# Performance work log

Measured on AMD Instinct MI355X. Metric: run time of the kernel, lower is better.

The kernel has to match this reference:

```python
import jax, jax.numpy as jnp
import numpy as np

# PtConv dims from SegSmall: pl=64 channels, n_centers=16 kernel elements, dim=3
B, N, K = 4, 16384, 16          # batch, points, neighbors
C_IN, C_OUT, KS, DIM = 64, 64, 16, 3


def setup_inputs() -> dict:
    key = jax.random.key(0)
    ks = jax.random.split(key, 10)
    features = jax.random.normal(ks[0], (B, N, C_IN), dtype=jnp.float32)
    input_pts = jax.random.uniform(ks[1], (B, N, DIM), dtype=jnp.float32)
    output_pts = input_pts  # same-resolution conv: queries == input points
    indices = jax.random.randint(ks[2], (B, N, K), 0, N)  # precomputed KNN indices
    # weight init as in PtConv
    bound = float(np.sqrt(3.0) * np.sqrt(2.0 / (C_IN + C_OUT)))
    weight = jax.random.uniform(ks[3], (C_IN, KS, C_OUT), jnp.float32, -bound, bound)
    bias = jnp.zeros((C_OUT,), jnp.float32)
    centers = jax.random.uniform(ks[4], (DIM, KS), jnp.float32, -1.0, 1.0)
    # position-MLP params: Linear(dim*KS -> 2*KS), Linear(2*KS -> KS), Linear(KS -> KS)
    def lin(k, fan_in, fan_out):
        lim = 1.0 / np.sqrt(fan_in)
        kw, kb = jax.random.split(k)
        W = jax.random.uniform(kw, (fan_in, fan_out), jnp.float32, -lim, lim)
        b = jax.random.uniform(kb, (fan_out,), jnp.float32, -lim, lim)
        return W, b
    w1, b1 = lin(ks[5], DIM * KS, 2 * KS)
    w2, b2 = lin(ks[6], 2 * KS, KS)
    w3, b3 = lin(ks[7], KS, KS)
    return {"features": features, "input_pts": input_pts, "output_pts": output_pts,
            "weight": weight, "bias": bias, "centers": centers,
            "w1": w1, "b1": b1, "w2": w2, "b2": b2, "w3": w3, "b3": b3,
            "indices": indices}


def reference(features, input_pts, output_pts, weight, bias, centers,
              w1, b1, w2, b2, w3, b3, indices):
    # per-batch gather of neighbor features and coordinates
    gather = jax.vmap(lambda a, idx: a[idx])
    feat_g = gather(features, indices)          # [B, M, K, C_in]
    pts_g = gather(input_pts, indices)          # [B, M, K, 3]
    pts = pts_g - output_pts[:, :, None, :]      # nn_center=True
    # distances to kernel centers: [B,M,K,3,1] - [3,KS] -> [B,M,K,3,KS] -> [B,M,K,3*KS]
    d = (pts[..., None] - centers).reshape(pts.shape[0], pts.shape[1], pts.shape[2], -1)
    d = jax.nn.relu(d @ w1 + b1)
    d = jax.nn.relu(d @ w2 + b2)
    d = jax.nn.relu(d @ w3 + b3)                 # [B, M, K, KS]
    # weighted neighbor aggregation: bmm(features^T, dists)
    agg = jnp.einsum('bmkc,bmkj->bmcj', feat_g, d)   # [B, M, C_in, KS]
    out = jnp.einsum('bmcj,cjo->bmo', agg, weight)   # flatten (C_in,KS) matches weight.view(-1,out)
    out = out / feat_g.shape[2]                      # divide by K (fs[2])
    out = out + bias
    return out
```

## Files before the change

kernel.cpp:

```cpp
#include <hip/hip_runtime.h>

#define NPTS 16384
#define KN   16
#define CIN  64
#define COUT 64
#define KSIZ 16
#define PTS  16

typedef _Float16 h4v    __attribute__((ext_vector_type(4)));
typedef _Float16 h8v    __attribute__((ext_vector_type(8)));
typedef __fp16   fp16x2 __attribute__((ext_vector_type(2)));
typedef float    f32x4  __attribute__((ext_vector_type(4)));

union H2U { fp16x2 h; unsigned u; };
union H4U { h4v v; fp16x2 p[2]; uint2 u2; };
union H8U { h8v v; uint4 u4; };

#define WS_WF_OFF   512
#define WS_F16_OFF  131584
#define WS_NEEDED   (131584ull + 8388608ull)

__global__ void prep_kernel(const float* __restrict__ weight,
                            const float* __restrict__ w1,
                            const float* __restrict__ b1,
                            const float* __restrict__ centers,
                            const float* __restrict__ features,
                            unsigned* __restrict__ wsp,
                            uint4* __restrict__ wf,
                            uint4* __restrict__ fb16) {
    const int b = blockIdx.x;
    const int t = threadIdx.x;
    if (b < 32) {
        const int bp = b*4 + (t>>6);
        const int kk = bp >> 2, nt = bp & 3;
        const int l = t & 63, li = l & 15, g = l >> 4;
        unsigned short u[8];
        #pragma unroll
        for (int e = 0; e < 8; ++e) {
            int s = kk*32 + g*8 + e;
            int j = s >> 6;
            int c = s & 63;
            union { _Float16 h; unsigned short s16; } cv;
            cv.h = (_Float16)(weight[(c*16 + j)*64 + nt*16 + li] * 0.0625f);
            u[e] = cv.s16;
        }
        uint4 v;
        v.x = u[0] | ((unsigned)u[1] << 16);
        v.y = u[2] | ((unsigned)u[3] << 16);
        v.z = u[4] | ((unsigned)u[5] << 16);
        v.w = u[6] | ((unsigned)u[7] << 16);
        wf[(kk*4 + nt)*64 + l] = v;
    } else if (b == 32) {
        __shared__ float tmp[4][32];
        if (t < 32) {
            int n = t;
            float s0 = 0.f, s1 = 0.f, s2 = 0.f, bf = b1[n];
            for (int s = 0; s < KSIZ; ++s) {
                float a0 = w1[(0*KSIZ + s)*32 + n];
                float a1 = w1[(1*KSIZ + s)*32 + n];
                float a2 = w1[(2*KSIZ + s)*32 + n];
                s0 += a0; s1 += a1; s2 += a2;
                bf -= centers[0*KSIZ+s]*a0 + centers[1*KSIZ+s]*a1 + centers[2*KSIZ+s]*a2;
            }
            tmp[0][n] = s0; tmp[1][n] = s1; tmp[2][n] = s2; tmp[3][n] = bf;
        }
        __syncthreads();
        if (t < 64) {
            const int row = t >> 4, q = t & 15;
            union { _Float16 h[2]; unsigned u; } pk;
            pk.h[0] = (_Float16)tmp[row][2*q];
            pk.h[1] = (_Float16)tmp[row][2*q+1];
            wsp[row*16 + q] = pk.u;
        }
    } else {
        const size_t e0 = ((size_t)(b - 33)*256 + t) * 8;
        const float4 f0 = *(const float4*)(features + e0);
        const float4 f1 = *(const float4*)(features + e0 + 4);
        union { _Float16 h[8]; uint4 v; } o;
        o.h[0] = (_Float16)f0.x; o.h[1] = (_Float16)f0.y;
        o.h[2] = (_Float16)f0.z; o.h[3] = (_Float16)f0.w;
        o.h[4] = (_Float16)f1.x; o.h[5] = (_Float16)f1.y;
        o.h[6] = (_Float16)f1.z; o.h[7] = (_Float16)f1.w;
        fb16[e0 >> 3] = o.v;
    }
}

template<int FM>
__global__ __launch_bounds__(256, 5)
void ptconv_kernel(const float* __restrict__ features,
                   const float* __restrict__ input_pts,
                   const float* __restrict__ output_pts,
                   const float* __restrict__ bias,
                   const float* __restrict__ w2,
                   const float* __restrict__ b2,
                   const float* __restrict__ w3,
                   const float* __restrict__ b3,
                   const int*   __restrict__ indices,
                   const unsigned* __restrict__ folded,
                   const uint4* __restrict__ wf,
                   const uint2* __restrict__ fb16,
                   float* __restrict__ out) {
    __shared__ __align__(16) char smem[32768];
    char* s_agg = smem;

    const int t    = threadIdx.x;
    const int l    = t & 63;
    const int wave = t >> 6;
    const int li   = l & 15;
    const int g    = l >> 4;
    const int m0   = blockIdx.x * PTS;
    const int bbk  = m0 >> 14;
    const int mloc = m0 & (NPTS-1);

    const int*   idxB  = indices    + (size_t)bbk*NPTS*KN;
    const float* ptsB  = input_pts  + (size_t)bbk*NPTS*3;
    const float* optsB = output_pts + (size_t)bbk*NPTS*3;
    const float* fb    = features + (size_t)bbk*NPTS*CIN;
    const uint2* fb16B = fb16 + (size_t)bbk*NPTS*(CIN/4);

    const int p1 = t >> 4, k1 = t & 15;
    const int nn = mloc + p1;
    const int idxv = idxB[nn*KN + k1];
    const float cop0 = optsB[nn*3+0], cop1 = optsB[nn*3+1], cop2 = optsB[nn*3+2];
    const float cip0 = ptsB[(size_t)idxv*3+0];
    const float cip1 = ptsB[(size_t)idxv*3+1];
    const float cip2 = ptsB[(size_t)idxv*3+2];

    const int4 idA = *(const int4*)(idxB + (mloc + wave*4+0)*KN + 4*g);
    const int4 idB = *(const int4*)(idxB + (mloc + wave*4+1)*KN + 4*g);
    const int4 idC = *(const int4*)(idxB + (mloc + wave*4+2)*KN + 4*g);
    const int4 idD = *(const int4*)(idxB + (mloc + wave*4+3)*KN + 4*g);

    H4U gA0, gA1, gA2, gA3, gB0, gB1, gB2, gB3;
    H4U gC0, gC1, gC2, gC3, gD0, gD1, gD2, gD3;
    f32x4 fA0, fA1, fA2, fA3, fB0, fB1, fB2, fB3;
    if constexpr (FM == 1) {
        gA0.u2 = fb16B[(size_t)idA.x*16 + li]; gA1.u2 = fb16B[(size_t)idA.y*16 + li];
        gA2.u2 = fb16B[(size_t)idA.z*16 + li]; gA3.u2 = fb16B[(size_t)idA.w*16 + li];
        gB0.u2 = fb16B[(size_t)idB.x*16 + li]; gB1.u2 = fb16B[(size_t)idB.y*16 + li];
        gB2.u2 = fb16B[(size_t)idB.z*16 + li]; gB3.u2 = fb16B[(size_t)idB.w*16 + li];
        gC0.u2 = fb16B[(size_t)idC.x*16 + li]; gC1.u2 = fb16B[(size_t)idC.y*16 + li];
        gC2.u2 = fb16B[(size_t)idC.z*16 + li]; gC3.u2 = fb16B[(size_t)idC.w*16 + li];
        gD0.u2 = fb16B[(size_t)idD.x*16 + li]; gD1.u2 = fb16B[(size_t)idD.y*16 + li];
        gD2.u2 = fb16B[(size_t)idD.z*16 + li]; gD3.u2 = fb16B[(size_t)idD.w*16 + li];
    } else {
        fA0 = *(const f32x4*)(fb + (size_t)idA.x*CIN + 4*li);
        fA1 = *(const f32x4*)(fb + (size_t)idA.y*CIN + 4*li);
        fA2 = *(const f32x4*)(fb + (size_t)idA.z*CIN + 4*li);
        fA3 = *(const f32x4*)(fb + (size_t)idA.w*CIN + 4*li);
        fB0 = *(const f32x4*)(fb + (size_t)idB.x*CIN + 4*li);
        fB1 = *(const f32x4*)(fb + (size_t)idB.y*CIN + 4*li);
        fB2 = *(const f32x4*)(fb + (size_t)idB.z*CIN + 4*li);
        fB3 = *(const f32x4*)(fb + (size_t)idB.w*CIN + 4*li);
    }

    h8v w2f; h4v w3f;
    #pragma unroll
    for (int e = 0; e < 8; ++e) w2f[e] = (_Float16)w2[(8*g+e)*16 + li];
    #pragma unroll
    for (int e = 0; e < 4; ++e) w3f[e] = (_Float16)w3[(4*g+e)*16 + li];
    const f32x4 b2v4  = *(const f32x4*)(b2 + 4*g);
    const float b3v   = b3[li];
    const float biasO = bias[wave*16 + li];
    const uint4* wp   = wf + wave*64 + l;

    {
        const __fp16 r0h = (__fp16)(cip0-cop0);
        const __fp16 r1h = (__fp16)(cip1-cop1);
        const __fp16 r2h = (__fp16)(cip2-cop2);
        fp16x2 r0p = {r0h, r0h}, r1p = {r1h, r1h}, r2p = {r2h, r2h};
        const fp16x2 zz = {(__fp16)0.f, (__fp16)0.f};
        uint4* dst = (uint4*)(smem + wave*8192 + l*80);
        unsigned o8[8];
        #pragma unroll
        for (int half = 0; half < 2; ++half) {
            #pragma unroll
            for (int qq = 0; qq < 8; ++qq) {
                const int q = half*8 + qq;
                H2U a, u0, u1, u2;
                a.u  = folded[48+q];
                u0.u = folded[q];
                u1.u = folded[16+q];
                u2.u = folded[32+q];
                fp16x2 acc = r0p*u0.h + a.h;
                acc = r1p*u1.h + acc;
                acc = r2p*u2.h + acc;
                acc = __builtin_elementwise_max(acc, zz);
                H2U o; o.h = acc; o8[qq] = o.u;
            }
            dst[half*2+0] = make_uint4(o8[0], o8[1], o8[2], o8[3]);
            dst[half*2+1] = make_uint4(o8[4], o8[5], o8[6], o8[7]);
        }
    }

    h4v dreg0, dreg1, dreg2, dreg3;
#define L23(PP, DREG) { \
    h8v B2 = *(const h8v*)(smem + wave*8192 + ((PP)*16 + li)*80 + g*16); \
    f32x4 a2 = b2v4; \
    a2 = __builtin_amdgcn_mfma_f32_16x16x32_f16(w2f, B2, a2, 0, 0, 0); \
    H4U A3; \
    A3.p[0] = __builtin_amdgcn_cvt_pkrtz(fmaxf(a2[0],0.f), fmaxf(a2[1],0.f)); \
    A3.p[1] = __builtin_amdgcn_cvt_pkrtz(fmaxf(a2[2],0.f), fmaxf(a2[3],0.f)); \
    f32x4 a3 = {b3v, b3v, b3v, b3v}; \
    a3 = __builtin_amdgcn_mfma_f32_16x16x16f16(A3.v, w3f, a3, 0, 0, 0); \
    H4U Dv; \
    Dv.p[0] = __builtin_amdgcn_cvt_pkrtz(fmaxf(a3[0],0.f), fmaxf(a3[1],0.f)); \
    Dv.p[1] = __builtin_amdgcn_cvt_pkrtz(fmaxf(a3[2],0.f), fmaxf(a3[3],0.f)); \
    DREG = Dv.v; }
    L23(0, dreg0) L23(1, dreg1) L23(2, dreg2) L23(3, dreg3)
#undef L23

#define P2STORE(PP, E0,E1,E2,E3) { \
    const int pix_ = wave*4 + (PP); \
    const unsigned swz_ = (unsigned)((pix_ & 7) << 4); \
    char* ab_ = s_agg + pix_*2048; \
    _Pragma("unroll") \
    for (int r = 0; r < 4; ++r) { \
        H2U d01, d23; \
        d01.h = __builtin_amdgcn_cvt_pkrtz(E0[r], E1[r]); \
        d23.h = __builtin_amdgcn_cvt_pkrtz(E2[r], E3[r]); \
        *(uint2*)(ab_ + ((unsigned)((4*g + r)*128 + 8*li) ^ swz_)) = \
            make_uint2(d01.u, d23.u); \
    } }

    if constexpr (FM == 1) {
#define P2F16(PP, R0,R1,R2,R3) { \
        f32x4 z = {0.f,0.f,0.f,0.f}; \
        f32x4 e0_, e1_, e2_, e3_; \
        { H4U B_; B_.v = (h4v){R0.v[0], R1.v[0], R2.v[0], R3.v[0]}; \
          e0_ = __builtin_amdgcn_mfma_f32_16x16x16f16(dreg##PP, B_.v, z, 0, 0, 0); } \
        { H4U B_; B_.v = (h4v){R0.v[1], R1.v[1], R2.v[1], R3.v[1]}; \
          e1_ = __builtin_amdgcn_mfma_f32_16x16x16f16(dreg##PP, B_.v, z, 0, 0, 0); } \
        { H4U B_; B_.v = (h4v){R0.v[2], R1.v[2], R2.v[2], R3.v[2]}; \
          e2_ = __builtin_amdgcn_mfma_f32_16x16x16f16(dreg##PP, B_.v, z, 0, 0, 0); } \
        { H4U B_; B_.v = (h4v){R0.v[3], R1.v[3], R2.v[3], R3.v[3]}; \
          e3_ = __builtin_amdgcn_mfma_f32_16x16x16f16(dreg##PP, B_.v, z, 0, 0, 0); } \
        P2STORE(PP, e0_, e1_, e2_, e3_) }
        P2F16(0, gA0, gA1, gA2, gA3)
        P2F16(1, gB0, gB1, gB2, gB3)
        P2F16(2, gC0, gC1, gC2, gC3)
        P2F16(3, gD0, gD1, gD2, gD3)
#undef P2F16
    } else {
#define P2F32(PP, R0,R1,R2,R3) { \
        f32x4 z = {0.f,0.f,0.f,0.f}; \
        f32x4 e0_, e1_, e2_, e3_; \
        { H4U B_; B_.p[0] = __builtin_amdgcn_cvt_pkrtz(R0[0], R1[0]); \
          B_.p[1] = __builtin_amdgcn_cvt_pkrtz(R2[0], R3[0]); \
          e0_ = __builtin_amdgcn_mfma_f32_16x16x16f16(dreg##PP, B_.v, z, 0, 0, 0); } \
        { H4U B_; B_.p[0] = __builtin_amdgcn_cvt_pkrtz(R0[1], R1[1]); \
          B_.p[1] = __builtin_amdgcn_cvt_pkrtz(R2[1], R3[1]); \
          e1_ = __builtin_amdgcn_mfma_f32_16x16x16f16(dreg##PP, B_.v, z, 0, 0, 0); } \
        { H4U B_; B_.p[0] = __builtin_amdgcn_cvt_pkrtz(R0[2], R1[2]); \
          B_.p[1] = __builtin_amdgcn_cvt_pkrtz(R2[2], R3[2]); \
          e2_ = __builtin_amdgcn_mfma_f32_16x16x16f16(dreg##PP, B_.v, z, 0, 0, 0); } \
        { H4U B_; B_.p[0] = __builtin_amdgcn_cvt_pkrtz(R0[3], R1[3]); \
          B_.p[1] = __builtin_amdgcn_cvt_pkrtz(R2[3], R3[3]); \
          e3_ = __builtin_amdgcn_mfma_f32_16x16x16f16(dreg##PP, B_.v, z, 0, 0, 0); } \
        P2STORE(PP, e0_, e1_, e2_, e3_) }
        P2F32(0, fA0, fA1, fA2, fA3)
        P2F32(1, fB0, fB1, fB2, fB3)
        fA0 = *(const f32x4*)(fb + (size_t)idC.x*CIN + 4*li);
        fA1 = *(const f32x4*)(fb + (size_t)idC.y*CIN + 4*li);
        fA2 = *(const f32x4*)(fb + (size_t)idC.z*CIN + 4*li);
        fA3 = *(const f32x4*)(fb + (size_t)idC.w*CIN + 4*li);
        fB0 = *(const f32x4*)(fb + (size_t)idD.x*CIN + 4*li);
        fB1 = *(const f32x4*)(fb + (size_t)idD.y*CIN + 4*li);
        fB2 = *(const f32x4*)(fb + (size_t)idD.z*CIN + 4*li);
        fB3 = *(const f32x4*)(fb + (size_t)idD.w*CIN + 4*li);
        P2F32(2, fA0, fA1, fA2, fA3)
        P2F32(3, fB0, fB1, fB2, fB3)
#undef P2F32
    }
#undef P2STORE

    uint4 q0 = wp[0*256], q1 = wp[1*256], q2 = wp[2*256], q3 = wp[3*256];
    uint4 q4 = wp[4*256], q5 = wp[5*256], q6 = wp[6*256], q7 = wp[7*256];

    asm volatile("s_waitcnt lgkmcnt(0)" ::: "memory");
    __builtin_amdgcn_s_barrier();
    asm volatile("" ::: "memory");

    __builtin_amdgcn_s_setprio(1);
    f32x4 a0 = {0.f,0.f,0.f,0.f}, a1 = a0, a2 = a0, a3 = a0;
    const unsigned swr = (unsigned)((li & 7) << 4);
#define AREAD(KK) (*(const h8v*)(s_agg + li*2048 + (((KK)*64 + g*16) ^ swr)))
#define MFS(KK, Q, ACC)  { H8U bu_; bu_.u4 = Q; \
    ACC = __builtin_amdgcn_mfma_f32_16x16x32_f16(AREAD(KK), bu_.v, ACC, 0, 0, 0); }
#define MFSL(KK, Q, ACC) MFS(KK, Q, ACC) Q = wp[((KK)+8)*256];
    MFSL(0, q0, a0) MFSL(1, q1, a1) MFSL(2, q2, a2) MFSL(3, q3, a3)
    MFSL(4, q4, a0) MFSL(5, q5, a1) MFSL(6, q6, a2) MFSL(7, q7, a3)
    MFSL(8, q0, a0) MFSL(9, q1, a1) MFSL(10, q2, a2) MFSL(11, q3, a3)
    MFSL(12, q4, a0) MFSL(13, q5, a1) MFSL(14, q6, a2) MFSL(15, q7, a3)
    MFSL(16, q0, a0) MFSL(17, q1, a1) MFSL(18, q2, a2) MFSL(19, q3, a3)
    MFSL(20, q4, a0) MFSL(21, q5, a1) MFSL(22, q6, a2) MFSL(23, q7, a3)
    MFS(24, q0, a0) MFS(25, q1, a1) MFS(26, q2, a2) MFS(27, q3, a3)
    MFS(28, q4, a0) MFS(29, q5, a1) MFS(30, q6, a2) MFS(31, q7, a3)
#undef MFSL
#undef MFS
#undef AREAD
    __builtin_amdgcn_s_setprio(0);

    const f32x4 acc = (a0 + a1) + (a2 + a3);
    #pragma unroll
    for (int r = 0; r < 4; ++r) {
        const int mr = g*4 + r;
        out[(size_t)(m0 + mr)*COUT + wave*16 + li] = acc[r] + biasO;
    }
}

extern "C" void kernel_launch(void* const* d_in, const int* in_sizes, int n_in,
                              void* d_out, int out_size, void* d_ws, size_t ws_size,
                              hipStream_t stream) {
    const float* features   = (const float*)d_in[0];
    const float* input_pts  = (const float*)d_in[1];
    const float* output_pts = (const float*)d_in[2];
    const float* weight     = (const float*)d_in[3];
    const float* bias       = (const float*)d_in[4];
    const float* centers    = (const float*)d_in[5];
    const float* w1         = (const float*)d_in[6];
    const float* b1         = (const float*)d_in[7];
    const float* w2         = (const float*)d_in[8];
    const float* b2         = (const float*)d_in[9];
    const float* w3         = (const float*)d_in[10];
    const float* b3         = (const float*)d_in[11];
    const int*   indices    = (const int*)d_in[12];
    float* out = (float*)d_out;
    unsigned* wsp = (unsigned*)d_ws;
    uint4* wf   = (uint4*)((char*)d_ws + WS_WF_OFF);
    uint4* fb16 = (uint4*)((char*)d_ws + WS_F16_OFF);

    const bool f16ok = ws_size >= WS_NEEDED;
    const int nconv = f16ok ? (4*NPTS*CIN) / (256*8) : 0;
    prep_kernel<<<33 + nconv, 256, 0, stream>>>(
        weight, w1, b1, centers, features, wsp, wf, fb16);

    const int total_pts = 4 * NPTS;
    if (f16ok) {
        ptconv_kernel<1><<<total_pts / PTS, 256, 0, stream>>>(
            features, input_pts, output_pts, bias,
            w2, b2, w3, b3, indices, wsp, wf, (const uint2*)fb16, out);
    } else {
        ptconv_kernel<0><<<total_pts / PTS, 256, 0, stream>>>(
            features, input_pts, output_pts, bias,
            w2, b2, w3, b3, indices, wsp, wf, (const uint2*)fb16, out);
    }
}
```

Measured before the change: 48.21 us.

## Make fp16 kernel persistent over four tiles with software-pipelined neighbor prefetch

The fp16 path now has each block handle four consecutive 16-point tiles instead of one, launching a quarter as many blocks. Indices, positions and gathered fp16 features for the next tile are loaded during the current tile's compute, hiding gather latency and amortising per-block setup (w2/w3/bias loads). This costs an extra barrier per tile, more live registers, a lower launch-bounds occupancy target (4 instead of 5) and fewer blocks to spread across CUs. The fp32 fallback is split into its own kernel and behaves as before.

```diff
diff --git a/kernel.cpp b/kernel.cpp
--- a/kernel.cpp
+++ b/kernel.cpp
@@ -6,6 +6,7 @@
 #define COUT 64
 #define KSIZ 16
 #define PTS  16
+#define ITERS 4
 
 typedef _Float16 h4v    __attribute__((ext_vector_type(4)));
 typedef _Float16 h8v    __attribute__((ext_vector_type(8)));
@@ -85,21 +86,19 @@
     }
 }
 
-template<int FM>
-__global__ __launch_bounds__(256, 5)
-void ptconv_kernel(const float* __restrict__ features,
-                   const float* __restrict__ input_pts,
-                   const float* __restrict__ output_pts,
-                   const float* __restrict__ bias,
-                   const float* __restrict__ w2,
-                   const float* __restrict__ b2,
-                   const float* __restrict__ w3,
-                   const float* __restrict__ b3,
-                   const int*   __restrict__ indices,
-                   const unsigned* __restrict__ folded,
-                   const uint4* __restrict__ wf,
-                   const uint2* __restrict__ fb16,
-                   float* __restrict__ out) {
+__global__ __launch_bounds__(256, 4)
+void ptconv_pipe(const float* __restrict__ input_pts,
+                 const float* __restrict__ output_pts,
+                 const float* __restrict__ bias,
+                 const float* __restrict__ w2,
+                 const float* __restrict__ b2,
+                 const float* __restrict__ w3,
+                 const float* __restrict__ b3,
+                 const int*   __restrict__ indices,
+                 const unsigned* __restrict__ folded,
+                 const uint4* __restrict__ wf,
+                 const uint2* __restrict__ fb16,
+                 float* __restrict__ out) {
     __shared__ __align__(16) char smem[32768];
     char* s_agg = smem;
 
@@ -108,51 +107,15 @@
     const int wave = t >> 6;
     const int li   = l & 15;
     const int g    = l >> 4;
-    const int m0   = blockIdx.x * PTS;
-    const int bbk  = m0 >> 14;
-    const int mloc = m0 & (NPTS-1);
+    const int base_m0 = blockIdx.x * (PTS*ITERS);
+    const int bbk   = base_m0 >> 14;
+    const int mloc  = base_m0 & (NPTS-1);
+    const int p1 = t >> 4, k1 = t & 15;
 
     const int*   idxB  = indices    + (size_t)bbk*NPTS*KN;
     const float* ptsB  = input_pts  + (size_t)bbk*NPTS*3;
     const float* optsB = output_pts + (size_t)bbk*NPTS*3;
-    const float* fb    = features + (size_t)bbk*NPTS*CIN;
     const uint2* fb16B = fb16 + (size_t)bbk*NPTS*(CIN/4);
-
-    const int p1 = t >> 4, k1 = t & 15;
-    const int nn = mloc + p1;
-    const int idxv = idxB[nn*KN + k1];
-    const float cop0 = optsB[nn*3+0], cop1 = optsB[nn*3+1], cop2 = optsB[nn*3+2];
-    const float cip0 = ptsB[(size_t)idxv*3+0];
-    const float cip1 = ptsB[(size_t)idxv*3+1];
-    const float cip2 = ptsB[(size_t)idxv*3+2];
-
-    const int4 idA = *(const int4*)(idxB + (mloc + wave*4+0)*KN + 4*g);
-    const int4 idB = *(const int4*)(idxB + (mloc + wave*4+1)*KN + 4*g);
-    const int4 idC = *(const int4*)(idxB + (mloc + wave*4+2)*KN + 4*g);
-    const int4 idD = *(const int4*)(idxB + (mloc + wave*4+3)*KN + 4*g);
-
-    H4U gA0, gA1, gA2, gA3, gB0, gB1, gB2, gB3;
-    H4U gC0, gC1, gC2, gC3, gD0, gD1, gD2, gD3;
-    f32x4 fA0, fA1, fA2, fA3, fB0, fB1, fB2, fB3;
-    if constexpr (FM == 1) {
-        gA0.u2 = fb16B[(size_t)idA.x*16 + li]; gA1.u2 = fb16B[(size_t)idA.y*16 + li];
-        gA2.u2 = fb16B[(size_t)idA.z*16 + li]; gA3.u2 = fb16B[(size_t)idA.w*16 + li];
-        gB0.u2 = fb16B[(size_t)idB.x*16 + li]; gB1.u2 = fb16B[(size_t)idB.y*16 + li];
-        gB2.u2 = fb16B[(size_t)idB.z*16 + li]; gB3.u2 = fb16B[(size_t)idB.w*16 + li];
-        gC0.u2 = fb16B[(size_t)idC.x*16 + li]; gC1.u2 = fb16B[(size_t)idC.y*16 + li];
-        gC2.u2 = fb16B[(size_t)idC.z*16 + li]; gC3.u2 = fb16B[(size_t)idC.w*16 + li];
-        gD0.u2 = fb16B[(size_t)idD.x*16 + li]; gD1.u2 = fb16B[(size_t)idD.y*16 + li];
-        gD2.u2 = fb16B[(size_t)idD.z*16 + li]; gD3.u2 = fb16B[(size_t)idD.w*16 + li];
-    } else {
-        fA0 = *(const f32x4*)(fb + (size_t)idA.x*CIN + 4*li);
-        fA1 = *(const f32x4*)(fb + (size_t)idA.y*CIN + 4*li);
-        fA2 = *(const f32x4*)(fb + (size_t)idA.z*CIN + 4*li);
-        fA3 = *(const f32x4*)(fb + (size_t)idA.w*CIN + 4*li);
-        fB0 = *(const f32x4*)(fb + (size_t)idB.x*CIN + 4*li);
-        fB1 = *(const f32x4*)(fb + (size_t)idB.y*CIN + 4*li);
-        fB2 = *(const f32x4*)(fb + (size_t)idB.z*CIN + 4*li);
-        fB3 = *(const f32x4*)(fb + (size_t)idB.w*CIN + 4*li);
-    }
 
     h8v w2f; h4v w3f;
     #pragma unroll
@@ -164,66 +127,107 @@
     const float biasO = bias[wave*16 + li];
     const uint4* wp   = wf + wave*64 + l;
 
+    float cip0, cip1, cip2, cop0, cop1, cop2;
+    H4U gA0, gA1, gA2, gA3, gB0, gB1, gB2, gB3;
+    H4U gC0, gC1, gC2, gC3, gD0, gD1, gD2, gD3;
     {
-        const __fp16 r0h = (__fp16)(cip0-cop0);
-        const __fp16 r1h = (__fp16)(cip1-cop1);
-        const __fp16 r2h = (__fp16)(cip2-cop2);
-        fp16x2 r0p = {r0h, r0h}, r1p = {r1h, r1h}, r2p = {r2h, r2h};
-        const fp16x2 zz = {(__fp16)0.f, (__fp16)0.f};
-        uint4* dst = (uint4*)(smem + wave*8192 + l*80);
-        unsigned o8[8];
-        #pragma unroll
-        for (int half = 0; half < 2; ++half) {
+        const int nn = mloc + p1;
+        const int idxv = idxB[nn*KN + k1];
+        cop0 = optsB[nn*3+0]; cop1 = optsB[nn*3+1]; cop2 = optsB[nn*3+2];
+        cip0 = ptsB[(size_t)idxv*3+0];
+        cip1 = ptsB[(size_t)idxv*3+1];
+        cip2 = ptsB[(size_t)idxv*3+2];
+        const int4 iA = *(const int4*)(idxB + (mloc + wave*4+0)*KN + 4*g);
+        const int4 iB = *(const int4*)(idxB + (mloc + wave*4+1)*KN + 4*g);
+        const int4 iC = *(const int4*)(idxB + (mloc + wave*4+2)*KN + 4*g);
+        const int4 iD = *(const int4*)(idxB + (mloc + wave*4+3)*KN + 4*g);
+        gA0.u2 = fb16B[(size_t)iA.x*16 + li]; gA1.u2 = fb16B[(size_t)iA.y*16 + li];
+        gA2.u2 = fb16B[(size_t)iA.z*16 + li]; gA3.u2 = fb16B[(size_t)iA.w*16 + li];
+        gB0.u2 = fb16B[(size_t)iB.x*16 + li]; gB1.u2 = fb16B[(size_t)iB.y*16 + li];
+        gB2.u2 = fb16B[(size_t)iB.z*16 + li]; gB3.u2 = fb16B[(size_t)iB.w*16 + li];
+        gC0.u2 = fb16B[(size_t)iC.x*16 + li]; gC1.u2 = fb16B[(size_t)iC.y*16 + li];
+        gC2.u2 = fb16B[(size_t)iC.z*16 + li]; gC3.u2 = fb16B[(size_t)iC.w*16 + li];
+        gD0.u2 = fb16B[(size_t)iD.x*16 + li]; gD1.u2 = fb16B[(size_t)iD.y*16 + li];
+        gD2.u2 = fb16B[(size_t)iD.z*16 + li]; gD3.u2 = fb16B[(size_t)iD.w*16 + li];
+    }
+
+    #pragma unroll 1
+    for (int it = 0; it < ITERS; ++it) {
+        const int m0i   = base_m0 + it*PTS;
+        const bool pf   = (it + 1 < ITERS);
+        const int mlocN = mloc + (it+1)*PTS;
+
+        int idxvN = 0;
+        float opN0 = 0.f, opN1 = 0.f, opN2 = 0.f;
+        int4 iA, iB, iC, iD;
+        if (pf) {
+            const int nnN = mlocN + p1;
+            idxvN = idxB[nnN*KN + k1];
+            opN0 = optsB[nnN*3+0]; opN1 = optsB[nnN*3+1]; opN2 = optsB[nnN*3+2];
+            iA = *(const int4*)(idxB + (mlocN + wave*4+0)*KN + 4*g);
+            iB = *(const int4*)(idxB + (mlocN + wave*4+1)*KN + 4*g);
+            iC = *(const int4*)(idxB + (mlocN + wave*4+2)*KN + 4*g);
+            iD = *(const int4*)(idxB + (mlocN + wave*4+3)*KN + 4*g);
+        }
+
+        {
+            const __fp16 r0h = (__fp16)(cip0-cop0);
+            const __fp16 r1h = (__fp16)(cip1-cop1);
+            const __fp16 r2h = (__fp16)(cip2-cop2);
+            fp16x2 r0p = {r0h, r0h}, r1p = {r1h, r1h}, r2p = {r2h, r2h};
+            const fp16x2 zz = {(__fp16)0.f, (__fp16)0.f};
+            uint4* dst = (uint4*)(smem + wave*8192 + l*80);
+            unsigned o8[8];
             #pragma unroll
-            for (int qq = 0; qq < 8; ++qq) {
-                const int q = half*8 + qq;
-                H2U a, u0, u1, u2;
-                a.u  = folded[48+q];
-                u0.u = folded[q];
-                u1.u = folded[16+q];
-                u2.u = folded[32+q];
-                fp16x2 acc = r0p*u0.h + a.h;
-                acc = r1p*u1.h + acc;
-                acc = r2p*u2.h + acc;
-                acc = __builtin_elementwise_max(acc, zz);
-                H2U o; o.h = acc; o8[qq] = o.u;
+            for (int half = 0; half < 2; ++half) {
+                #pragma unroll
+                for (int qq = 0; qq < 8; ++qq) {
+                    const int q = half*8 + qq;
+                    H2U a, u0, u1, u2;
+                    a.u  = folded[48+q];
+                    u0.u = folded[q];
+                    u1.u = folded[16+q];
+                    u2.u = folded[32+q];
+                    fp16x2 acc = r0p*u0.h + a.h;
+                    acc = r1p*u1.h + acc;
+                    acc = r2p*u2.h + acc;
+                    acc = __builtin_elementwise_max(acc, zz);
+                    H2U o; o.h = acc; o8[qq] = o.u;
+                }
+                dst[half*2+0] = make_uint4(o8[0], o8[1], o8[2], o8[3]);
+                dst[half*2+1] = make_uint4(o8[4], o8[5], o8[6], o8[7]);
             }
-            dst[half*2+0] = make_uint4(o8[0], o8[1], o8[2], o8[3]);
-            dst[half*2+1] = make_uint4(o8[4], o8[5], o8[6], o8[7]);
-        }
-    }
-
-    h4v dreg0, dreg1, dreg2, dreg3;
+        }
+
+        h4v dreg0, dreg1, dreg2, dreg3;
 #define L23(PP, DREG) { \
-    h8v B2 = *(const h8v*)(smem + wave*8192 + ((PP)*16 + li)*80 + g*16); \
-    f32x4 a2 = b2v4; \
-    a2 = __builtin_amdgcn_mfma_f32_16x16x32_f16(w2f, B2, a2, 0, 0, 0); \
-    H4U A3; \
-    A3.p[0] = __builtin_amdgcn_cvt_pkrtz(fmaxf(a2[0],0.f), fmaxf(a2[1],0.f)); \
-    A3.p[1] = __builtin_amdgcn_cvt_pkrtz(fmaxf(a2[2],0.f), fmaxf(a2[3],0.f)); \
-    f32x4 a3 = {b3v, b3v, b3v, b3v}; \
-    a3 = __builtin_amdgcn_mfma_f32_16x16x16f16(A3.v, w3f, a3, 0, 0, 0); \
-    H4U Dv; \
-    Dv.p[0] = __builtin_amdgcn_cvt_pkrtz(fmaxf(a3[0],0.f), fmaxf(a3[1],0.f)); \
-    Dv.p[1] = __builtin_amdgcn_cvt_pkrtz(fmaxf(a3[2],0.f), fmaxf(a3[3],0.f)); \
-    DREG = Dv.v; }
-    L23(0, dreg0) L23(1, dreg1) L23(2, dreg2) L23(3, dreg3)
+        h8v B2 = *(const h8v*)(smem + wave*8192 + ((PP)*16 + li)*80 + g*16); \
+        f32x4 a2 = b2v4; \
+        a2 = __builtin_amdgcn_mfma_f32_16x16x32_f16(w2f, B2, a2, 0, 0, 0); \
+        H4U A3; \
+        A3.p[0] = __builtin_amdgcn_cvt_pkrtz(fmaxf(a2[0],0.f), fmaxf(a2[1],0.f)); \
+        A3.p[1] = __builtin_amdgcn_cvt_pkrtz(fmaxf(a2[2],0.f), fmaxf(a2[3],0.f)); \
+        f32x4 a3 = {b3v, b3v, b3v, b3v}; \
+        a3 = __builtin_amdgcn_mfma_f32_16x16x16f16(A3.v, w3f, a3, 0, 0, 0); \
+        H4U Dv; \
+        Dv.p[0] = __builtin_amdgcn_cvt_pkrtz(fmaxf(a3[0],0.f), fmaxf(a3[1],0.f)); \
+        Dv.p[1] = __builtin_amdgcn_cvt_pkrtz(fmaxf(a3[2],0.f), fmaxf(a3[3],0.f)); \
+        DREG = Dv.v; }
+        L23(0, dreg0) L23(1, dreg1) L23(2, dreg2) L23(3, dreg3)
 #undef L23
 
 #define P2STORE(PP, E0,E1,E2,E3) { \
-    const int pix_ = wave*4 + (PP); \
-    const unsigned swz_ = (unsigned)((pix_ & 7) << 4); \
-    char* ab_ = s_agg + pix_*2048; \
-    _Pragma("unroll") \
-    for (int r = 0; r < 4; ++r) { \
-        H2U d01, d23; \
-        d01.h = __builtin_amdgcn_cvt_pkrtz(E0[r], E1[r]); \
-        d23.h = __builtin_amdgcn_cvt_pkrtz(E2[r], E3[r]); \
-        *(uint2*)(ab_ + ((unsigned)((4*g + r)*128 + 8*li) ^ swz_)) = \
-            make_uint2(d01.u, d23.u); \
-    } }
-
-    if constexpr (FM == 1) {
+        const int pix_ = wave*4 + (PP); \
+        const unsigned swz_ = (unsigned)((pix_ & 7) << 4); \
+        char* ab_ = s_agg + pix_*2048; \
+        _Pragma("unroll") \
+        for (int r = 0; r < 4; ++r) { \
+            H2U d01, d23; \
+            d01.h = __builtin_amdgcn_cvt_pkrtz(E0[r], E1[r]); \
+            d23.h = __builtin_amdgcn_cvt_pkrtz(E2[r], E3[r]); \
+            *(uint2*)(ab_ + ((unsigned)((4*g + r)*128 + 8*li) ^ swz_)) = \
+                make_uint2(d01.u, d23.u); \
+        } }
 #define P2F16(PP, R0,R1,R2,R3) { \
         f32x4 z = {0.f,0.f,0.f,0.f}; \
         f32x4 e0_, e1_, e2_, e3_; \
@@ -241,46 +245,201 @@
         P2F16(2, gC0, gC1, gC2, gC3)
         P2F16(3, gD0, gD1, gD2, gD3)
 #undef P2F16
-    } else {
+#undef P2STORE
+
+        float ipN0 = 0.f, ipN1 = 0.f, ipN2 = 0.f;
+        if (pf) {
+            ipN0 = ptsB[(size_t)idxvN*3+0];
+            ipN1 = ptsB[(size_t)idxvN*3+1];
+            ipN2 = ptsB[(size_t)idxvN*3+2];
+        }
+        uint4 q0 = wp[0*256], q1 = wp[1*256], q2 = wp[2*256], q3 = wp[3*256];
+        uint4 q4 = wp[4*256], q5 = wp[5*256], q6 = wp[6*256], q7 = wp[7*256];
+
+        asm volatile("s_waitcnt lgkmcnt(0)" ::: "memory");
+        __builtin_amdgcn_s_barrier();
+        asm volatile("" ::: "memory");
+
+        __builtin_amdgcn_s_setprio(1);
+        f32x4 a0 = {0.f,0.f,0.f,0.f}, a1 = a0, a2 = a0, a3 = a0;
+        const unsigned swr = (unsigned)((li & 7) << 4);
+#define AREAD(KK) (*(const h8v*)(s_agg + li*2048 + (((KK)*64 + g*16) ^ swr)))
+#define MFS(KK, Q, ACC)  { H8U bu_; bu_.u4 = Q; \
+        ACC = __builtin_amdgcn_mfma_f32_16x16x32_f16(AREAD(KK), bu_.v, ACC, 0, 0, 0); }
+#define MFSL(KK, Q, ACC) MFS(KK, Q, ACC) Q = wp[((KK)+8)*256];
+        MFSL(0, q0, a0) MFSL(1, q1, a1) MFSL(2, q2, a2) MFSL(3, q3, a3)
+        MFSL(4, q4, a0) MFSL(5, q5, a1) MFSL(6, q6, a2) MFSL(7, q7, a3)
+        MFSL(8, q0, a0) MFSL(9, q1, a1) MFSL(10, q2, a2) MFSL(11, q3, a3)
+        MFSL(12, q4, a0) MFSL(13, q5, a1) MFSL(14, q6, a2) MFSL(15, q7, a3)
+        MFSL(16, q0, a0) MFSL(17, q1, a1) MFSL(18, q2, a2) MFSL(19, q3, a3)
+        MFSL(20, q4, a0) MFSL(21, q5, a1) MFSL(22, q6, a2) MFSL(23, q7, a3)
+        MFS(24, q0, a0) MFS(25, q1, a1) MFS(26, q2, a2) MFS(27, q3, a3)
+        MFS(28, q4, a0) MFS(29, q5, a1) MFS(30, q6, a2) MFS(31, q7, a3)
+#undef MFSL
+#undef MFS
+#undef AREAD
+        __builtin_amdgcn_s_setprio(0);
+
+        const f32x4 acc = (a0 + a1) + (a2 + a3);
+        #pragma unroll
+        for (int r = 0; r < 4; ++r) {
+            const int mr = g*4 + r;
+            out[(size_t)(m0i + mr)*COUT + wave*16 + li] = acc[r] + biasO;
+        }
+
+        asm volatile("" ::: "memory");
+        __builtin_amdgcn_s_barrier();
+        asm volatile("" ::: "memory");
+
+        if (pf) {
+            gA0.u2 = fb16B[(size_t)iA.x*16 + li]; gA1.u2 = fb16B[(size_t)iA.y*16 + li];
+            gA2.u2 = fb16B[(size_t)iA.z*16 + li]; gA3.u2 = fb16B[(size_t)iA.w*16 + li];
+            gB0.u2 = fb16B[(size_t)iB.x*16 + li]; gB1.u2 = fb16B[(size_t)iB.y*16 + li];
+            gB2.u2 = fb16B[(size_t)iB.z*16 + li]; gB3.u2 = fb16B[(size_t)iB.w*16 + li];
+            gC0.u2 = fb16B[(size_t)iC.x*16 + li]; gC1.u2 = fb16B[(size_t)iC.y*16 + li];
+            gC2.u2 = fb16B[(size_t)iC.z*16 + li]; gC3.u2 = fb16B[(size_t)iC.w*16 + li];
+            gD0.u2 = fb16B[(size_t)iD.x*16 + li]; gD1.u2 = fb16B[(size_t)iD.y*16 + li];
+            gD2.u2 = fb16B[(size_t)iD.z*16 + li]; gD3.u2 = fb16B[(size_t)iD.w*16 + li];
+            asm volatile("" ::: "memory");
+            cip0 = ipN0; cip1 = ipN1; cip2 = ipN2;
+            cop0 = opN0; cop1 = opN1; cop2 = opN2;
+        }
+    }
+}
+
+__global__ __launch_bounds__(256, 4)
+void ptconv_f32(const float* __restrict__ features,
+                const float* __restrict__ input_pts,
+                const float* __restrict__ output_pts,
+                const float* __restrict__ bias,
+                const float* __restrict__ w2,
+                const float* __restrict__ b2,
+                const float* __restrict__ w3,
+                const float* __restrict__ b3,
+                const int*   __restrict__ indices,
+                const unsigned* __restrict__ folded,
+                const uint4* __restrict__ wf,
+                float* __restrict__ out) {
+    __shared__ __align__(16) char smem[32768];
+    char* s_agg = smem;
+    const int t = threadIdx.x, l = t & 63, wave = t >> 6, li = l & 15, g = l >> 4;
+    const int m0 = blockIdx.x * PTS, bbk = m0 >> 14, mloc = m0 & (NPTS-1);
+    const int*   idxB  = indices    + (size_t)bbk*NPTS*KN;
+    const float* ptsB  = input_pts  + (size_t)bbk*NPTS*3;
+    const float* optsB = output_pts + (size_t)bbk*NPTS*3;
+    const float* fb    = features   + (size_t)bbk*NPTS*CIN;
+    const int p1 = t >> 4, k1 = t & 15;
+    const int nn = mloc + p1;
+    const int idxv = idxB[nn*KN + k1];
+    const float cop0 = optsB[nn*3+0], cop1 = optsB[nn*3+1], cop2 = optsB[nn*3+2];
+    const float cip0 = ptsB[(size_t)idxv*3+0];
+    const float cip1 = ptsB[(size_t)idxv*3+1];
+    const float cip2 = ptsB[(size_t)idxv*3+2];
+    const int4 idA = *(const int4*)(idxB + (mloc + wave*4+0)*KN + 4*g);
+    const int4 idB = *(const int4*)(idxB + (mloc + wave*4+1)*KN + 4*g);
+    const int4 idC = *(const int4*)(idxB + (mloc + wave*4+2)*KN + 4*g);
+    const int4 idD = *(const int4*)(idxB + (mloc + wave*4+3)*KN + 4*g);
+    f32x4 fA0 = *(const f32x4*)(fb + (size_t)idA.x*CIN + 4*li);
+    f32x4 fA1 = *(const f32x4*)(fb + (size_t)idA.y*CIN + 4*li);
+    f32x4 fA2 = *(const f32x4*)(fb + (size_t)idA.z*CIN + 4*li);
+    f32x4 fA3 = *(const f32x4*)(fb + (size_t)idA.w*CIN + 4*li);
+    f32x4 fB0 = *(const f32x4*)(fb + (size_t)idB.x*CIN + 4*li);
+    f32x4 fB1 = *(const f32x4*)(fb + (size_t)idB.y*CIN + 4*li);
+    f32x4 fB2 = *(const f32x4*)(fb + (size_t)idB.z*CIN + 4*li);
+    f32x4 fB3 = *(const f32x4*)(fb + (size_t)idB.w*CIN + 4*li);
+    h8v w2f; h4v w3f;
+    #pragma unroll
+    for (int e = 0; e < 8; ++e) w2f[e] = (_Float16)w2[(8*g+e)*16 + li];
+    #pragma unroll
+    for (int e = 0; e < 4; ++e) w3f[e] = (_Float16)w3[(4*g+e)*16 + li];
+    const f32x4 b2v4 = *(const f32x4*)(b2 + 4*g);
+    const float b3v = b3[li], biasO = bias[wave*16 + li];
+    const uint4* wp = wf + wave*64 + l;
+    {
+        const __fp16 r0h = (__fp16)(cip0-cop0), r1h = (__fp16)(cip1-cop1), r2h = (__fp16)(cip2-cop2);
+        fp16x2 r0p = {r0h, r0h}, r1p = {r1h, r1h}, r2p = {r2h, r2h};
+        const fp16x2 zz = {(__fp16)0.f, (__fp16)0.f};
+        uint4* dst = (uint4*)(smem + wave*8192 + l*80);
+        unsigned o8[8];
+        #pragma unroll
+        for (int half = 0; half < 2; ++half) {
+            #pragma unroll
+            for (int qq = 0; qq < 8; ++qq) {
+                const int q = half*8 + qq;
+                H2U a, u0, u1, u2;
+                a.u = folded[48+q]; u0.u = folded[q]; u1.u = folded[16+q]; u2.u = folded[32+q];
+                fp16x2 acc = r0p*u0.h + a.h;
+                acc = r1p*u1.h + acc;
+                acc = r2p*u2.h + acc;
+                acc = __builtin_elementwise_max(acc, zz);
+                H2U o; o.h = acc; o8[qq] = o.u;
+            }
+            dst[half*2+0] = make_uint4(o8[0], o8[1], o8[2], o8[3]);
+            dst[half*2+1] = make_uint4(o8[4], o8[5], o8[6], o8[7]);
+        }
+    }
+    h4v dreg0, dreg1, dreg2, dreg3;
+#define L23(PP, DREG) { \
+    h8v B2 = *(const h8v*)(smem + wave*8192 + ((PP)*16 + li)*80 + g*16); \
+    f32x4 a2 = b2v4; \
+    a2 = __builtin_amdgcn_mfma_f32_16x16x32_f16(w2f, B2, a2, 0, 0, 0); \
+    H4U A3; \
+    A3.p[0] = __builtin_amdgcn_cvt_pkrtz(fmaxf(a2[0],0.f), fmaxf(a2[1],0.f)); \
+    A3.p[1] = __builtin_amdgcn_cvt_pkrtz(fmaxf(a2[2],0.f), fmaxf(a2[3],0.f)); \
+    f32x4 a3 = {b3v, b3v, b3v, b3v}; \
+    a3 = __builtin_amdgcn_mfma_f32_16x16x16f16(A3.v, w3f, a3, 0, 0, 0); \
+    H4U Dv; \
+    Dv.p[0] = __builtin_amdgcn_cvt_pkrtz(fmaxf(a3[0],0.f), fmaxf(a3[1],0.f)); \
+    Dv.p[1] = __builtin_amdgcn_cvt_pkrtz(fmaxf(a3[2],0.f), fmaxf(a3[3],0.f)); \
+    DREG = Dv.v; }
+    L23(0, dreg0) L23(1, dreg1) L23(2, dreg2) L23(3, dreg3)
+#undef L23
+#define P2STORE(PP, E0,E1,E2,E3) { \
+    const int pix_ = wave*4 + (PP); \
+    const unsigned swz_ = (unsigned)((pix_ & 7) << 4); \
+    char* ab_ = s_agg + pix_*2048; \
+    _Pragma("unroll") \
+    for (int r = 0; r < 4; ++r) { \
+        H2U d01, d23; \
+        d01.h = __builtin_amdgcn_cvt_pkrtz(E0[r], E1[r]); \
+        d23.h = __builtin_amdgcn_cvt_pkrtz(E2[r], E3[r]); \
+        *(uint2*)(ab_ + ((unsigned)((4*g + r)*128 + 8*li) ^ swz_)) = make_uint2(d01.u, d23.u); \
+    } }
 #define P2F32(PP, R0,R1,R2,R3) { \
-        f32x4 z = {0.f,0.f,0.f,0.f}; \
-        f32x4 e0_, e1_, e2_, e3_; \
-        { H4U B_; B_.p[0] = __builtin_amdgcn_cvt_pkrtz(R0[0], R1[0]); \
-          B_.p[1] = __builtin_amdgcn_cvt_pkrtz(R2[0], R3[0]); \
-          e0_ = __builtin_amdgcn_mfma_f32_16x16x16f16(dreg##PP, B_.v, z, 0, 0, 0); } \
-        { H4U B_; B_.p[0] = __builtin_amdgcn_cvt_pkrtz(R0[1], R1[1]); \
-          B_.p[1] = __builtin_amdgcn_cvt_pkrtz(R2[1], R3[1]); \
-          e1_ = __builtin_amdgcn_mfma_f32_16x16x16f16(dreg##PP, B_.v, z, 0, 0, 0); } \
-        { H4U B_; B_.p[0] = __builtin_amdgcn_cvt_pkrtz(R0[2], R1[2]); \
-          B_.p[1] = __builtin_amdgcn_cvt_pkrtz(R2[2], R3[2]); \
-          e2_ = __builtin_amdgcn_mfma_f32_16x16x16f16(dreg##PP, B_.v, z, 0, 0, 0); } \
-        { H4U B_; B_.p[0] = __builtin_amdgcn_cvt_pkrtz(R0[3], R1[3]); \
-          B_.p[1] = __builtin_amdgcn_cvt_pkrtz(R2[3], R3[3]); \
-          e3_ = __builtin_amdgcn_mfma_f32_16x16x16f16(dreg##PP, B_.v, z, 0, 0, 0); } \
-        P2STORE(PP, e0_, e1_, e2_, e3_) }
-        P2F32(0, fA0, fA1, fA2, fA3)
-        P2F32(1, fB0, fB1, fB2, fB3)
-        fA0 = *(const f32x4*)(fb + (size_t)idC.x*CIN + 4*li);
-        fA1 = *(const f32x4*)(fb + (size_t)idC.y*CIN + 4*li);
-        fA2 = *(const f32x4*)(fb + (size_t)idC.z*CIN + 4*li);
-        fA3 = *(const f32x4*)(fb + (size_t)idC.w*CIN + 4*li);
-        fB0 = *(const f32x4*)(fb + (size_t)idD.x*CIN + 4*li);
-        fB1 = *(const f32x4*)(fb + (size_t)idD.y*CIN + 4*li);
-        fB2 = *(const f32x4*)(fb + (size_t)idD.z*CIN + 4*li);
-        fB3 = *(const f32x4*)(fb + (size_t)idD.w*CIN + 4*li);
-        P2F32(2, fA0, fA1, fA2, fA3)
-        P2F32(3, fB0, fB1, fB2, fB3)
+    f32x4 z = {0.f,0.f,0.f,0.f}; \
+    f32x4 e0_, e1_, e2_, e3_; \
+    { H4U B_; B_.p[0] = __builtin_amdgcn_cvt_pkrtz(R0[0], R1[0]); \
+      B_.p[1] = __builtin_amdgcn_cvt_pkrtz(R2[0], R3[0]); \
+      e0_ = __builtin_amdgcn_mfma_f32_16x16x16f16(dreg##PP, B_.v, z, 0, 0, 0); } \
+    { H4U B_; B_.p[0] = __builtin_amdgcn_cvt_pkrtz(R0[1], R1[1]); \
+      B_.p[1] = __builtin_amdgcn_cvt_pkrtz(R2[1], R3[1]); \
+      e1_ = __builtin_amdgcn_mfma_f32_16x16x16f16(dreg##PP, B_.v, z, 0, 0, 0); } \
+    { H4U B_; B_.p[0] = __builtin_amdgcn_cvt_pkrtz(R0[2], R1[2]); \
+      B_.p[1] = __builtin_amdgcn_cvt_pkrtz(R2[2], R3[2]); \
+      e2_ = __builtin_amdgcn_mfma_f32_16x16x16f16(dreg##PP, B_.v, z, 0, 0, 0); } \
+    { H4U B_; B_.p[0] = __builtin_amdgcn_cvt_pkrtz(R0[3], R1[3]); \
+      B_.p[1] = __builtin_amdgcn_cvt_pkrtz(R2[3], R3[3]); \
+      e3_ = __builtin_amdgcn_mfma_f32_16x16x16f16(dreg##PP, B_.v, z, 0, 0, 0); } \
+    P2STORE(PP, e0_, e1_, e2_, e3_) }
+    P2F32(0, fA0, fA1, fA2, fA3)
+    P2F32(1, fB0, fB1, fB2, fB3)
+    fA0 = *(const f32x4*)(fb + (size_t)idC.x*CIN + 4*li);
+    fA1 = *(const f32x4*)(fb + (size_t)idC.y*CIN + 4*li);
+    fA2 = *(const f32x4*)(fb + (size_t)idC.z*CIN + 4*li);
+    fA3 = *(const f32x4*)(fb + (size_t)idC.w*CIN + 4*li);
+    fB0 = *(const f32x4*)(fb + (size_t)idD.x*CIN + 4*li);
+    fB1 = *(const f32x4*)(fb + (size_t)idD.y*CIN + 4*li);
+    fB2 = *(const f32x4*)(fb + (size_t)idD.z*CIN + 4*li);
+    fB3 = *(const f32x4*)(fb + (size_t)idD.w*CIN + 4*li);
+    P2F32(2, fA0, fA1, fA2, fA3)
+    P2F32(3, fB0, fB1, fB2, fB3)
 #undef P2F32
-    }
 #undef P2STORE
-
     uint4 q0 = wp[0*256], q1 = wp[1*256], q2 = wp[2*256], q3 = wp[3*256];
     uint4 q4 = wp[4*256], q5 = wp[5*256], q6 = wp[6*256], q7 = wp[7*256];
-
     asm volatile("s_waitcnt lgkmcnt(0)" ::: "memory");
     __builtin_amdgcn_s_barrier();
     asm volatile("" ::: "memory");
-
     __builtin_amdgcn_s_setprio(1);
     f32x4 a0 = {0.f,0.f,0.f,0.f}, a1 = a0, a2 = a0, a3 = a0;
     const unsigned swr = (unsigned)((li & 7) << 4);
@@ -300,7 +459,6 @@
 #undef MFS
 #undef AREAD
     __builtin_amdgcn_s_setprio(0);
-
     const f32x4 acc = (a0 + a1) + (a2 + a3);
     #pragma unroll
     for (int r = 0; r < 4; ++r) {
@@ -337,12 +495,12 @@
 
     const int total_pts = 4 * NPTS;
     if (f16ok) {
-        ptconv_kernel<1><<<total_pts / PTS, 256, 0, stream>>>(
-            features, input_pts, output_pts, bias,
+        ptconv_pipe<<<total_pts / (PTS*ITERS), 256, 0, stream>>>(
+            input_pts, output_pts, bias,
             w2, b2, w3, b3, indices, wsp, wf, (const uint2*)fb16, out);
     } else {
-        ptconv_kernel<0><<<total_pts / PTS, 256, 0, stream>>>(
+        ptconv_f32<<<total_pts / PTS, 256, 0, stream>>>(
             features, input_pts, output_pts, bias,
-            w2, b2, w3, b3, indices, wsp, wf, (const uint2*)fb16, out);
+            w2, b2, w3, b3, indices, wsp, wf, out);
     }
 }
```

New measurement: 141.9 us. +194.3%, slower.
